# Performance work log

Hardware: AMD Instinct MI355X
Metric: run time of the kernel (lower is better)

The kernel has to match this reference:

```python
import jax, jax.numpy as jnp
import numpy as np

HIDDEN = 1024
INTER = 2048
NUM_EXPERTS = 8
TOPK = 2
STD = 0.02


def setup_inputs() -> dict:
    key = jax.random.key(0)
    k1, k2, k3, k4 = jax.random.split(key, 4)
    return {
        "hidden_states": jax.random.normal(k1, (1, 2048, HIDDEN), dtype=jnp.float32),
        "w1": jax.random.normal(k2, (NUM_EXPERTS, 2 * INTER, HIDDEN), dtype=jnp.float32) * STD,
        "w2": jax.random.normal(k3, (NUM_EXPERTS, HIDDEN, INTER), dtype=jnp.float32) * STD,
        "router_w": jax.random.normal(k4, (NUM_EXPERTS, HIDDEN), dtype=jnp.float32) * STD,
    }


def reference(hidden_states, w1, w2, router_w):
    # renormalize=False (the torch forward's default)
    orig_shape = hidden_states.shape
    dtype = hidden_states.dtype
    x = hidden_states.reshape(-1, orig_shape[-1])          # [T, H]
    E = w1.shape[0]

    gating = x @ router_w.T                                 # [T, E]
    probs = jax.nn.softmax(gating.astype(jnp.float32), axis=-1)
    topk_w, sel = jax.lax.top_k(probs, TOPK)                # [T, K]
    topk_w = topk_w.astype(dtype)

    # Per-(token, expert) combine weight; equivalent to the dispatch/sort/
    # grouped-GEMM/index_add path since unselected experts get weight 0.
    combine = (jax.nn.one_hot(sel, E, dtype=dtype) * topk_w[..., None]).sum(axis=1)  # [T, E]

    h = jnp.einsum('td,eid->tei', x, w1)                    # [T, E, 2*INTER]
    gate = jax.nn.silu(h[..., :INTER])
    y = h[..., INTER:] * gate                               # [T, E, INTER]
    out = jnp.einsum('tei,ehi,te->th', y, w2, combine)      # [T, H]
    return out.reshape(orig_shape)
```

## Files before the change

### kernel.cpp

```cpp
#include <hip/hip_runtime.h>
#include <hip/hip_bf16.h>
#include <math.h>

#define T_TOKENS 2048
#define HID 1024
#define INTER 2048
#define NE 8

typedef __attribute__((ext_vector_type(8))) __bf16 bf16x8;
typedef __attribute__((ext_vector_type(4))) __bf16 bf16x4;
typedef __attribute__((ext_vector_type(4))) float f32x4;

#define WS_COUNTS   0u
#define WS_OFFSETS  64u
#define WS_SEL      128u
#define WS_SELW     16512u
#define WS_ROWTOK   32896u
#define WS_ROWW     49280u
#define WS_TOKROWS  65664u
#define WS_XB       131072u
#define WS_Y        (131072u + 4194304u)
#define WS_Z        (131072u + 4194304u + 16777216u)

__device__ __forceinline__ void gload_lds16(const void* g, void* l) {
    __builtin_amdgcn_global_load_lds(
        (const __attribute__((address_space(1))) unsigned int*)g,
        (__attribute__((address_space(3))) unsigned int*)l, 16, 0, 0);
}

__device__ __forceinline__ bf16x8 cvt8(float4 a, float4 b) {
    bf16x8 r;
    r[0] = (__bf16)a.x; r[1] = (__bf16)a.y; r[2] = (__bf16)a.z; r[3] = (__bf16)a.w;
    r[4] = (__bf16)b.x; r[5] = (__bf16)b.y; r[6] = (__bf16)b.z; r[7] = (__bf16)b.w;
    return r;
}

__device__ __forceinline__ bf16x8 ldsfrag(const __bf16* base, int row, int c4) {
    return *(const bf16x8*)((const char*)base + row * 128 + ((c4 ^ (row & 7)) << 4));
}

__global__ __launch_bounds__(256) void moe_router(
    const float* __restrict__ x, const float* __restrict__ rw,
    int* __restrict__ counts, int* __restrict__ sel, float* __restrict__ selw,
    __bf16* __restrict__ xb)
{
    int wave = threadIdx.x >> 6;
    int lane = threadIdx.x & 63;
    int t = blockIdx.x * 4 + wave;
    if (t >= T_TOKENS) return;

    const float4* x4  = (const float4*)x + (size_t)t * (HID / 4);
    const float4* rw4 = (const float4*)rw;

    float acc[NE];
#pragma unroll
    for (int e = 0; e < NE; ++e) acc[e] = 0.f;
#pragma unroll
    for (int q = 0; q < 4; ++q) {
        int idx = q * 64 + lane;
        float4 xv = x4[idx];
        bf16x4 c;
        c[0] = (__bf16)xv.x; c[1] = (__bf16)xv.y; c[2] = (__bf16)xv.z; c[3] = (__bf16)xv.w;
        *(bf16x4*)(xb + (size_t)t * HID + idx * 4) = c;
#pragma unroll
        for (int e = 0; e < NE; ++e) {
            float4 rv = rw4[e * (HID / 4) + idx];
            acc[e] += xv.x * rv.x + xv.y * rv.y + xv.z * rv.z + xv.w * rv.w;
        }
    }
#pragma unroll
    for (int off = 32; off; off >>= 1)
#pragma unroll
        for (int e = 0; e < NE; ++e) acc[e] += __shfl_xor(acc[e], off, 64);

    if (lane == 0) {
        float m = acc[0];
#pragma unroll
        for (int e = 1; e < NE; ++e) m = fmaxf(m, acc[e]);
        float p[NE], s = 0.f;
#pragma unroll
        for (int e = 0; e < NE; ++e) { p[e] = expf(acc[e] - m); s += p[e]; }
        float inv = 1.f / s;
        int i0 = 0;
#pragma unroll
        for (int e = 1; e < NE; ++e) if (p[e] > p[i0]) i0 = e;
        int i1 = (i0 == 0) ? 1 : 0;
#pragma unroll
        for (int e = 0; e < NE; ++e) if (e != i0 && p[e] > p[i1]) i1 = e;
        sel[t * 2 + 0] = i0; selw[t * 2 + 0] = p[i0] * inv;
        sel[t * 2 + 1] = i1; selw[t * 2 + 1] = p[i1] * inv;
        atomicAdd(&counts[i0], 1);
        atomicAdd(&counts[i1], 1);
    }
}

__global__ __launch_bounds__(256) void moe_scan_assign(
    const int* __restrict__ counts, int* __restrict__ offsets,
    const int* __restrict__ sel, const float* __restrict__ selw,
    int* __restrict__ row_token, float* __restrict__ row_w,
    int* __restrict__ token_rows)
{
    __shared__ int soff[NE];
    __shared__ int scur[NE];
    if (threadIdx.x == 0) {
        int off = 0;
        for (int e = 0; e < NE; ++e) { soff[e] = off; off += counts[e]; }
    }
    if (threadIdx.x < NE) scur[threadIdx.x] = 0;
    __syncthreads();
    if (threadIdx.x < NE) offsets[threadIdx.x] = soff[threadIdx.x];
    for (int t = threadIdx.x; t < T_TOKENS; t += 256) {
#pragma unroll
        for (int k = 0; k < 2; ++k) {
            int e = sel[t * 2 + k];
            int slot = atomicAdd(&scur[e], 1);
            int r = soff[e] + slot;
            row_token[r] = t;
            row_w[r] = selw[t * 2 + k];
            token_rows[t * 2 + k] = r;
        }
    }
}

__global__ __launch_bounds__(256, 2) void moe_gemm1(
    const __bf16* __restrict__ xb, const float* __restrict__ w1,
    const int* __restrict__ row_token, const int* __restrict__ counts,
    const int* __restrict__ offsets, __bf16* __restrict__ y)
{
    int e = blockIdx.z;
    int cnt = counts[e];
    int row0 = blockIdx.y * 128;
    if (row0 >= cnt) return;
    int col0 = blockIdx.x * 64;
    int base = offsets[e];

    __shared__ __bf16 As[2][128 * 64];
    __shared__ __bf16 Bg[2][64 * 64];
    __shared__ __bf16 Bu[2][64 * 64];

    int tid = threadIdx.x;
    int lane = tid & 63;
    int wid = tid >> 6;
    int c4 = lane & 7;

    const __bf16* srcA[4];
    int dstA[4];
#pragma unroll
    for (int i = 0; i < 4; ++i) {
        int ii = wid * 4 + i;
        int r = ii * 8 + (lane >> 3);
        int rl = row0 + r; if (rl > cnt - 1) rl = cnt - 1;
        int tok = row_token[base + rl];
        srcA[i] = xb + (size_t)tok * HID + ((c4 ^ (r & 7)) << 3);
        dstA[i] = ii * 1024 + lane * 16;
    }
    const float* srcBg[2]; const float* srcBu[2]; int offB[2];
    int tc4 = tid & 7;
#pragma unroll
    for (int p = 0; p < 2; ++p) {
        int rb = p * 32 + (tid >> 3);
        srcBg[p] = w1 + ((size_t)e * 2 * INTER + col0 + rb) * HID + (tc4 << 3);
        srcBu[p] = srcBg[p] + (size_t)INTER * HID;
        offB[p] = rb * 128 + ((tc4 ^ (rb & 7)) << 4);
    }

#pragma unroll
    for (int i = 0; i < 4; ++i) gload_lds16(srcA[i], (char*)As[0] + dstA[i]);
#pragma unroll
    for (int p = 0; p < 2; ++p) {
        float4 g0 = *(const float4*)(srcBg[p]);
        float4 g1 = *(const float4*)(srcBg[p] + 4);
        float4 u0 = *(const float4*)(srcBu[p]);
        float4 u1 = *(const float4*)(srcBu[p] + 4);
        *(bf16x8*)((char*)Bg[0] + offB[p]) = cvt8(g0, g1);
        *(bf16x8*)((char*)Bu[0] + offB[p]) = cvt8(u0, u1);
    }
    __syncthreads();

    int wr = (wid >> 1) * 64, wc = (wid & 1) * 32;
    f32x4 ag[4][2] = {}, au[4][2] = {};

    for (int t = 0; t < 16; ++t) {
        int cur = t & 1;
        float4 g0[2], g1[2], u0[2], u1[2];
        bool pre = (t < 15);
        if (pre) {
            int k0 = (t + 1) * 64;
#pragma unroll
            for (int i = 0; i < 4; ++i)
                gload_lds16(srcA[i] + k0, (char*)As[cur ^ 1] + dstA[i]);
#pragma unroll
            for (int p = 0; p < 2; ++p) {
                g0[p] = *(const float4*)(srcBg[p] + k0);
                g1[p] = *(const float4*)(srcBg[p] + k0 + 4);
                u0[p] = *(const float4*)(srcBu[p] + k0);
                u1[p] = *(const float4*)(srcBu[p] + k0 + 4);
            }
        }
        const __bf16* Ab = As[cur];
        const __bf16* Bgb = Bg[cur];
        const __bf16* Bub = Bu[cur];
#pragma unroll
        for (int ks = 0; ks < 2; ++ks) {
            int kc4 = ks * 4 + (lane >> 4);
            bf16x8 a[4], bg[2], bu[2];
#pragma unroll
            for (int m = 0; m < 4; ++m) a[m] = ldsfrag(Ab, wr + m * 16 + (lane & 15), kc4);
#pragma unroll
            for (int n = 0; n < 2; ++n) {
                bg[n] = ldsfrag(Bgb, wc + n * 16 + (lane & 15), kc4);
                bu[n] = ldsfrag(Bub, wc + n * 16 + (lane & 15), kc4);
            }
#pragma unroll
            for (int m = 0; m < 4; ++m)
#pragma unroll
                for (int n = 0; n < 2; ++n) {
                    ag[m][n] = __builtin_amdgcn_mfma_f32_16x16x32_bf16(a[m], bg[n], ag[m][n], 0, 0, 0);
                    au[m][n] = __builtin_amdgcn_mfma_f32_16x16x32_bf16(a[m], bu[n], au[m][n], 0, 0, 0);
                }
        }
        if (pre) {
#pragma unroll
            for (int p = 0; p < 2; ++p) {
                *(bf16x8*)((char*)Bg[cur ^ 1] + offB[p]) = cvt8(g0[p], g1[p]);
                *(bf16x8*)((char*)Bu[cur ^ 1] + offB[p]) = cvt8(u0[p], u1[p]);
            }
        }
        __syncthreads();
    }

#pragma unroll
    for (int m = 0; m < 4; ++m) {
#pragma unroll
        for (int j = 0; j < 4; ++j) {
            int rl = wr + m * 16 + ((lane >> 4) << 2) + j;
            if (row0 + rl >= cnt) continue;
            size_t yrow = (size_t)(base + row0 + rl) * INTER;
#pragma unroll
            for (int n = 0; n < 2; ++n) {
                float g = ag[m][n][j], u = au[m][n][j];
                float s = g / (1.f + __expf(-g));
                y[yrow + col0 + wc + n * 16 + (lane & 15)] = (__bf16)(s * u);
            }
        }
    }
}

__global__ __launch_bounds__(256, 3) void moe_gemm2(
    const __bf16* __restrict__ y, const float* __restrict__ w2,
    const float* __restrict__ row_w, const int* __restrict__ counts,
    const int* __restrict__ offsets, float* __restrict__ z)
{
    int e = blockIdx.z;
    int cnt = counts[e];
    int row0 = blockIdx.y * 128;
    if (row0 >= cnt) return;
    int col0 = blockIdx.x * 64;
    int base = offsets[e];

    __shared__ __bf16 As[2][128 * 64];
    __shared__ __bf16 Bs[2][64 * 64];

    int tid = threadIdx.x;
    int lane = tid & 63;
    int wid = tid >> 6;
    int c4 = lane & 7;

    const __bf16* srcA[4];
    int dstA[4];
#pragma unroll
    for (int i = 0; i < 4; ++i) {
        int ii = wid * 4 + i;
        int r = ii * 8 + (lane >> 3);
        int rl = row0 + r; if (rl > cnt - 1) rl = cnt - 1;
        srcA[i] = y + (size_t)(base + rl) * INTER + ((c4 ^ (r & 7)) << 3);
        dstA[i] = ii * 1024 + lane * 16;
    }
    const float* srcB[2]; int offB[2];
    int tc4 = tid & 7;
#pragma unroll
    for (int p = 0; p < 2; ++p) {
        int rb = p * 32 + (tid >> 3);
        srcB[p] = w2 + ((size_t)e * HID + col0 + rb) * INTER + (tc4 << 3);
        offB[p] = rb * 128 + ((tc4 ^ (rb & 7)) << 4);
    }

#pragma unroll
    for (int i = 0; i < 4; ++i) gload_lds16(srcA[i], (char*)As[0] + dstA[i]);
#pragma unroll
    for (int p = 0; p < 2; ++p) {
        float4 b0 = *(const float4*)(srcB[p]);
        float4 b1 = *(const float4*)(srcB[p] + 4);
        *(bf16x8*)((char*)Bs[0] + offB[p]) = cvt8(b0, b1);
    }
    __syncthreads();

    int wr = (wid >> 1) * 64, wc = (wid & 1) * 32;
    f32x4 acc[4][2] = {};

    for (int t = 0; t < 32; ++t) {
        int cur = t & 1;
        float4 b0[2], b1[2];
        bool pre = (t < 31);
        if (pre) {
            int k0 = (t + 1) * 64;
#pragma unroll
            for (int i = 0; i < 4; ++i)
                gload_lds16(srcA[i] + k0, (char*)As[cur ^ 1] + dstA[i]);
#pragma unroll
            for (int p = 0; p < 2; ++p) {
                b0[p] = *(const float4*)(srcB[p] + k0);
                b1[p] = *(const float4*)(srcB[p] + k0 + 4);
            }
        }
        const __bf16* Ab = As[cur];
        const __bf16* Bb = Bs[cur];
#pragma unroll
        for (int ks = 0; ks < 2; ++ks) {
            int kc4 = ks * 4 + (lane >> 4);
            bf16x8 a[4], b[2];
#pragma unroll
            for (int m = 0; m < 4; ++m) a[m] = ldsfrag(Ab, wr + m * 16 + (lane & 15), kc4);
#pragma unroll
            for (int n = 0; n < 2; ++n) b[n] = ldsfrag(Bb, wc + n * 16 + (lane & 15), kc4);
#pragma unroll
            for (int m = 0; m < 4; ++m)
#pragma unroll
                for (int n = 0; n < 2; ++n)
                    acc[m][n] = __builtin_amdgcn_mfma_f32_16x16x32_bf16(a[m], b[n], acc[m][n], 0, 0, 0);
        }
        if (pre) {
#pragma unroll
            for (int p = 0; p < 2; ++p)
                *(bf16x8*)((char*)Bs[cur ^ 1] + offB[p]) = cvt8(b0[p], b1[p]);
        }
        __syncthreads();
    }

#pragma unroll
    for (int m = 0; m < 4; ++m) {
#pragma unroll
        for (int j = 0; j < 4; ++j) {
            int rl = wr + m * 16 + ((lane >> 4) << 2) + j;
            if (row0 + rl >= cnt) continue;
            float wgt = row_w[base + row0 + rl];
            size_t zrow = (size_t)(base + row0 + rl) * HID;
#pragma unroll
            for (int n = 0; n < 2; ++n)
                z[zrow + col0 + wc + n * 16 + (lane & 15)] = acc[m][n][j] * wgt;
        }
    }
}

__global__ __launch_bounds__(256) void moe_combine(
    const float* __restrict__ z, const int* __restrict__ token_rows,
    float* __restrict__ out)
{
    int total = T_TOKENS * (HID / 4);
    for (int idx = blockIdx.x * 256 + threadIdx.x; idx < total; idx += gridDim.x * 256) {
        int t  = idx >> 8;
        int h4 = idx & 255;
        int r0 = token_rows[t * 2 + 0];
        int r1 = token_rows[t * 2 + 1];
        const float4* z4 = (const float4*)z;
        float4 a = z4[(size_t)r0 * 256 + h4];
        float4 b = z4[(size_t)r1 * 256 + h4];
        float4 o = {a.x + b.x, a.y + b.y, a.z + b.z, a.w + b.w};
        ((float4*)out)[(size_t)t * 256 + h4] = o;
    }
}

extern "C" void kernel_launch(void* const* d_in, const int* in_sizes, int n_in,
                              void* d_out, int out_size, void* d_ws, size_t ws_size,
                              hipStream_t stream) {
    const float* x  = (const float*)d_in[0];
    const float* w1 = (const float*)d_in[1];
    const float* w2 = (const float*)d_in[2];
    const float* rw = (const float*)d_in[3];
    float* out = (float*)d_out;

    char* ws = (char*)d_ws;
    int*    counts     = (int*)(ws + WS_COUNTS);
    int*    offsets    = (int*)(ws + WS_OFFSETS);
    int*    sel        = (int*)(ws + WS_SEL);
    float*  selw       = (float*)(ws + WS_SELW);
    int*    row_token  = (int*)(ws + WS_ROWTOK);
    float*  row_w      = (float*)(ws + WS_ROWW);
    int*    token_rows = (int*)(ws + WS_TOKROWS);
    __bf16* xb         = (__bf16*)(ws + WS_XB);
    __bf16* y          = (__bf16*)(ws + WS_Y);
    float*  z          = (float*)(ws + WS_Z);

    hipMemsetAsync(ws, 0, 128, stream);

    moe_router<<<T_TOKENS / 4, 256, 0, stream>>>(x, rw, counts, sel, selw, xb);
    moe_scan_assign<<<1, 256, 0, stream>>>(counts, offsets, sel, selw,
                                           row_token, row_w, token_rows);
    moe_gemm1<<<dim3(INTER / 64, 16, NE), 256, 0, stream>>>(
        xb, w1, row_token, counts, offsets, y);
    moe_gemm2<<<dim3(HID / 64, 16, NE), 256, 0, stream>>>(
        y, w2, row_w, counts, offsets, z);
    moe_combine<<<1024, 256, 0, stream>>>(z, token_rows, out);
}
```

Before: 407.7 us.

## Fuse combine into gemm2 via atomics, split-K gemm2, halve K tile

```diff
diff --git a/kernel.cpp b/kernel.cpp
--- a/kernel.cpp
+++ b/kernel.cpp
@@ -17,10 +17,8 @@
 #define WS_SELW     16512u
 #define WS_ROWTOK   32896u
 #define WS_ROWW     49280u
-#define WS_TOKROWS  65664u
 #define WS_XB       131072u
 #define WS_Y        (131072u + 4194304u)
-#define WS_Z        (131072u + 4194304u + 16777216u)
 
 __device__ __forceinline__ void gload_lds16(const void* g, void* l) {
     __builtin_amdgcn_global_load_lds(
@@ -35,8 +33,9 @@
     return r;
 }
 
-__device__ __forceinline__ bf16x8 ldsfrag(const __bf16* base, int row, int c4) {
-    return *(const bf16x8*)((const char*)base + row * 128 + ((c4 ^ (row & 7)) << 4));
+__device__ __forceinline__ bf16x8 ldsfrag(const __bf16* base, int row, int g) {
+    return *(const bf16x8*)((const char*)base + row * 64 +
+                            ((g ^ ((row >> 1) & 3)) << 4));
 }
 
 __global__ __launch_bounds__(256) void moe_router(
@@ -97,8 +96,7 @@
 __global__ __launch_bounds__(256) void moe_scan_assign(
     const int* __restrict__ counts, int* __restrict__ offsets,
     const int* __restrict__ sel, const float* __restrict__ selw,
-    int* __restrict__ row_token, float* __restrict__ row_w,
-    int* __restrict__ token_rows)
+    int* __restrict__ row_token, float* __restrict__ row_w)
 {
     __shared__ int soff[NE];
     __shared__ int scur[NE];
@@ -117,12 +115,11 @@
             int r = soff[e] + slot;
             row_token[r] = t;
             row_w[r] = selw[t * 2 + k];
-            token_rows[t * 2 + k] = r;
-        }
-    }
-}
-
-__global__ __launch_bounds__(256, 2) void moe_gemm1(
+        }
+    }
+}
+
+__global__ __launch_bounds__(256, 4) void moe_gemm1(
     const __bf16* __restrict__ xb, const float* __restrict__ w1,
     const int* __restrict__ row_token, const int* __restrict__ counts,
     const int* __restrict__ offsets, __bf16* __restrict__ y)
@@ -134,82 +131,72 @@
     int col0 = blockIdx.x * 64;
     int base = offsets[e];
 
-    __shared__ __bf16 As[2][128 * 64];
-    __shared__ __bf16 Bg[2][64 * 64];
-    __shared__ __bf16 Bu[2][64 * 64];
+    __shared__ __bf16 As[2][128 * 32];
+    __shared__ __bf16 Bg[2][64 * 32];
+    __shared__ __bf16 Bu[2][64 * 32];
 
     int tid = threadIdx.x;
     int lane = tid & 63;
     int wid = tid >> 6;
-    int c4 = lane & 7;
-
-    const __bf16* srcA[4];
-    int dstA[4];
-#pragma unroll
-    for (int i = 0; i < 4; ++i) {
-        int ii = wid * 4 + i;
-        int r = ii * 8 + (lane >> 3);
+    int gq = tid & 3;
+    int sw = (tid >> 3) & 3;
+
+    const __bf16* srcA[2];
+    int dstA[2];
+#pragma unroll
+    for (int i = 0; i < 2; ++i) {
+        int r = i * 64 + (tid >> 2);
         int rl = row0 + r; if (rl > cnt - 1) rl = cnt - 1;
         int tok = row_token[base + rl];
-        srcA[i] = xb + (size_t)tok * HID + ((c4 ^ (r & 7)) << 3);
-        dstA[i] = ii * 1024 + lane * 16;
-    }
-    const float* srcBg[2]; const float* srcBu[2]; int offB[2];
-    int tc4 = tid & 7;
-#pragma unroll
-    for (int p = 0; p < 2; ++p) {
-        int rb = p * 32 + (tid >> 3);
-        srcBg[p] = w1 + ((size_t)e * 2 * INTER + col0 + rb) * HID + (tc4 << 3);
-        srcBu[p] = srcBg[p] + (size_t)INTER * HID;
-        offB[p] = rb * 128 + ((tc4 ^ (rb & 7)) << 4);
-    }
-
-#pragma unroll
-    for (int i = 0; i < 4; ++i) gload_lds16(srcA[i], (char*)As[0] + dstA[i]);
-#pragma unroll
-    for (int p = 0; p < 2; ++p) {
-        float4 g0 = *(const float4*)(srcBg[p]);
-        float4 g1 = *(const float4*)(srcBg[p] + 4);
-        float4 u0 = *(const float4*)(srcBu[p]);
-        float4 u1 = *(const float4*)(srcBu[p] + 4);
-        *(bf16x8*)((char*)Bg[0] + offB[p]) = cvt8(g0, g1);
-        *(bf16x8*)((char*)Bu[0] + offB[p]) = cvt8(u0, u1);
+        srcA[i] = xb + (size_t)tok * HID + ((gq ^ sw) << 3);
+        dstA[i] = i * 4096 + tid * 16;
+    }
+    int rb = tid >> 2;
+    const float* srcBg = w1 + ((size_t)e * 2 * INTER + col0 + rb) * HID + (gq << 3);
+    const float* srcBu = srcBg + (size_t)INTER * HID;
+    int offB = rb * 64 + ((gq ^ sw) << 4);
+
+#pragma unroll
+    for (int i = 0; i < 2; ++i) gload_lds16(srcA[i], (char*)As[0] + dstA[i]);
+    {
+        float4 g0 = *(const float4*)(srcBg);
+        float4 g1 = *(const float4*)(srcBg + 4);
+        float4 u0 = *(const float4*)(srcBu);
+        float4 u1 = *(const float4*)(srcBu + 4);
+        *(bf16x8*)((char*)Bg[0] + offB) = cvt8(g0, g1);
+        *(bf16x8*)((char*)Bu[0] + offB) = cvt8(u0, u1);
     }
     __syncthreads();
 
     int wr = (wid >> 1) * 64, wc = (wid & 1) * 32;
     f32x4 ag[4][2] = {}, au[4][2] = {};
 
-    for (int t = 0; t < 16; ++t) {
+    for (int t = 0; t < 32; ++t) {
         int cur = t & 1;
-        float4 g0[2], g1[2], u0[2], u1[2];
-        bool pre = (t < 15);
+        float4 g0, g1, u0, u1;
+        bool pre = (t < 31);
         if (pre) {
-            int k0 = (t + 1) * 64;
-#pragma unroll
-            for (int i = 0; i < 4; ++i)
+            int k0 = (t + 1) * 32;
+#pragma unroll
+            for (int i = 0; i < 2; ++i)
                 gload_lds16(srcA[i] + k0, (char*)As[cur ^ 1] + dstA[i]);
-#pragma unroll
-            for (int p = 0; p < 2; ++p) {
-                g0[p] = *(const float4*)(srcBg[p] + k0);
-                g1[p] = *(const float4*)(srcBg[p] + k0 + 4);
-                u0[p] = *(const float4*)(srcBu[p] + k0);
-                u1[p] = *(const float4*)(srcBu[p] + k0 + 4);
-            }
+            g0 = *(const float4*)(srcBg + k0);
+            g1 = *(const float4*)(srcBg + k0 + 4);
+            u0 = *(const float4*)(srcBu + k0);
+            u1 = *(const float4*)(srcBu + k0 + 4);
         }
         const __bf16* Ab = As[cur];
         const __bf16* Bgb = Bg[cur];
         const __bf16* Bub = Bu[cur];
-#pragma unroll
-        for (int ks = 0; ks < 2; ++ks) {
-            int kc4 = ks * 4 + (lane >> 4);
+        {
+            int kg = lane >> 4;
             bf16x8 a[4], bg[2], bu[2];
 #pragma unroll
-            for (int m = 0; m < 4; ++m) a[m] = ldsfrag(Ab, wr + m * 16 + (lane & 15), kc4);
+            for (int m = 0; m < 4; ++m) a[m] = ldsfrag(Ab, wr + m * 16 + (lane & 15), kg);
 #pragma unroll
             for (int n = 0; n < 2; ++n) {
-                bg[n] = ldsfrag(Bgb, wc + n * 16 + (lane & 15), kc4);
-                bu[n] = ldsfrag(Bub, wc + n * 16 + (lane & 15), kc4);
+                bg[n] = ldsfrag(Bgb, wc + n * 16 + (lane & 15), kg);
+                bu[n] = ldsfrag(Bub, wc + n * 16 + (lane & 15), kg);
             }
 #pragma unroll
             for (int m = 0; m < 4; ++m)
@@ -220,11 +207,8 @@
                 }
         }
         if (pre) {
-#pragma unroll
-            for (int p = 0; p < 2; ++p) {
-                *(bf16x8*)((char*)Bg[cur ^ 1] + offB[p]) = cvt8(g0[p], g1[p]);
-                *(bf16x8*)((char*)Bu[cur ^ 1] + offB[p]) = cvt8(u0[p], u1[p]);
-            }
+            *(bf16x8*)((char*)Bg[cur ^ 1] + offB) = cvt8(g0, g1);
+            *(bf16x8*)((char*)Bu[cur ^ 1] + offB) = cvt8(u0, u1);
         }
         __syncthreads();
     }
@@ -246,52 +230,48 @@
     }
 }
 
-__global__ __launch_bounds__(256, 3) void moe_gemm2(
+__global__ __launch_bounds__(256, 4) void moe_gemm2(
     const __bf16* __restrict__ y, const float* __restrict__ w2,
-    const float* __restrict__ row_w, const int* __restrict__ counts,
-    const int* __restrict__ offsets, float* __restrict__ z)
+    const float* __restrict__ row_w, const int* __restrict__ row_token,
+    const int* __restrict__ counts, const int* __restrict__ offsets,
+    float* __restrict__ out)
 {
     int e = blockIdx.z;
     int cnt = counts[e];
-    int row0 = blockIdx.y * 128;
+    int row0 = (blockIdx.y >> 1) * 128;
     if (row0 >= cnt) return;
+    int kbase = (blockIdx.y & 1) * (INTER / 2);
     int col0 = blockIdx.x * 64;
     int base = offsets[e];
 
-    __shared__ __bf16 As[2][128 * 64];
-    __shared__ __bf16 Bs[2][64 * 64];
+    __shared__ __bf16 As[2][128 * 32];
+    __shared__ __bf16 Bs[2][64 * 32];
 
     int tid = threadIdx.x;
     int lane = tid & 63;
     int wid = tid >> 6;
-    int c4 = lane & 7;
-
-    const __bf16* srcA[4];
-    int dstA[4];
-#pragma unroll
-    for (int i = 0; i < 4; ++i) {
-        int ii = wid * 4 + i;
-        int r = ii * 8 + (lane >> 3);
+    int gq = tid & 3;
+    int sw = (tid >> 3) & 3;
+
+    const __bf16* srcA[2];
+    int dstA[2];
+#pragma unroll
+    for (int i = 0; i < 2; ++i) {
+        int r = i * 64 + (tid >> 2);
         int rl = row0 + r; if (rl > cnt - 1) rl = cnt - 1;
-        srcA[i] = y + (size_t)(base + rl) * INTER + ((c4 ^ (r & 7)) << 3);
-        dstA[i] = ii * 1024 + lane * 16;
-    }
-    const float* srcB[2]; int offB[2];
-    int tc4 = tid & 7;
-#pragma unroll
-    for (int p = 0; p < 2; ++p) {
-        int rb = p * 32 + (tid >> 3);
-        srcB[p] = w2 + ((size_t)e * HID + col0 + rb) * INTER + (tc4 << 3);
-        offB[p] = rb * 128 + ((tc4 ^ (rb & 7)) << 4);
-    }
-
-#pragma unroll
-    for (int i = 0; i < 4; ++i) gload_lds16(srcA[i], (char*)As[0] + dstA[i]);
-#pragma unroll
-    for (int p = 0; p < 2; ++p) {
-        float4 b0 = *(const float4*)(srcB[p]);
-        float4 b1 = *(const float4*)(srcB[p] + 4);
-        *(bf16x8*)((char*)Bs[0] + offB[p]) = cvt8(b0, b1);
+        srcA[i] = y + (size_t)(base + rl) * INTER + kbase + ((gq ^ sw) << 3);
+        dstA[i] = i * 4096 + tid * 16;
+    }
+    int rb = tid >> 2;
+    const float* srcB = w2 + ((size_t)e * HID + col0 + rb) * INTER + kbase + (gq << 3);
+    int offB = rb * 64 + ((gq ^ sw) << 4);
+
+#pragma unroll
+    for (int i = 0; i < 2; ++i) gload_lds16(srcA[i], (char*)As[0] + dstA[i]);
+    {
+        float4 b0 = *(const float4*)(srcB);
+        float4 b1 = *(const float4*)(srcB + 4);
+        *(bf16x8*)((char*)Bs[0] + offB) = cvt8(b0, b1);
     }
     __syncthreads();
 
@@ -300,29 +280,25 @@
 
     for (int t = 0; t < 32; ++t) {
         int cur = t & 1;
-        float4 b0[2], b1[2];
+        float4 b0, b1;
         bool pre = (t < 31);
         if (pre) {
-            int k0 = (t + 1) * 64;
-#pragma unroll
-            for (int i = 0; i < 4; ++i)
+            int k0 = (t + 1) * 32;
+#pragma unroll
+            for (int i = 0; i < 2; ++i)
                 gload_lds16(srcA[i] + k0, (char*)As[cur ^ 1] + dstA[i]);
-#pragma unroll
-            for (int p = 0; p < 2; ++p) {
-                b0[p] = *(const float4*)(srcB[p] + k0);
-                b1[p] = *(const float4*)(srcB[p] + k0 + 4);
-            }
+            b0 = *(const float4*)(srcB + k0);
+            b1 = *(const float4*)(srcB + k0 + 4);
         }
         const __bf16* Ab = As[cur];
         const __bf16* Bb = Bs[cur];
-#pragma unroll
-        for (int ks = 0; ks < 2; ++ks) {
-            int kc4 = ks * 4 + (lane >> 4);
+        {
+            int kg = lane >> 4;
             bf16x8 a[4], b[2];
 #pragma unroll
-            for (int m = 0; m < 4; ++m) a[m] = ldsfrag(Ab, wr + m * 16 + (lane & 15), kc4);
-#pragma unroll
-            for (int n = 0; n < 2; ++n) b[n] = ldsfrag(Bb, wc + n * 16 + (lane & 15), kc4);
+            for (int m = 0; m < 4; ++m) a[m] = ldsfrag(Ab, wr + m * 16 + (lane & 15), kg);
+#pragma unroll
+            for (int n = 0; n < 2; ++n) b[n] = ldsfrag(Bb, wc + n * 16 + (lane & 15), kg);
 #pragma unroll
             for (int m = 0; m < 4; ++m)
 #pragma unroll
@@ -330,9 +306,7 @@
                     acc[m][n] = __builtin_amdgcn_mfma_f32_16x16x32_bf16(a[m], b[n], acc[m][n], 0, 0, 0);
         }
         if (pre) {
-#pragma unroll
-            for (int p = 0; p < 2; ++p)
-                *(bf16x8*)((char*)Bs[cur ^ 1] + offB[p]) = cvt8(b0[p], b1[p]);
+            *(bf16x8*)((char*)Bs[cur ^ 1] + offB) = cvt8(b0, b1);
         }
         __syncthreads();
     }
@@ -344,29 +318,12 @@
             int rl = wr + m * 16 + ((lane >> 4) << 2) + j;
             if (row0 + rl >= cnt) continue;
             float wgt = row_w[base + row0 + rl];
-            size_t zrow = (size_t)(base + row0 + rl) * HID;
+            int tok = row_token[base + row0 + rl];
 #pragma unroll
             for (int n = 0; n < 2; ++n)
-                z[zrow + col0 + wc + n * 16 + (lane & 15)] = acc[m][n][j] * wgt;
-        }
-    }
-}
-
-__global__ __launch_bounds__(256) void moe_combine(
-    const float* __restrict__ z, const int* __restrict__ token_rows,
-    float* __restrict__ out)
-{
-    int total = T_TOKENS * (HID / 4);
-    for (int idx = blockIdx.x * 256 + threadIdx.x; idx < total; idx += gridDim.x * 256) {
-        int t  = idx >> 8;
-        int h4 = idx & 255;
-        int r0 = token_rows[t * 2 + 0];
-        int r1 = token_rows[t * 2 + 1];
-        const float4* z4 = (const float4*)z;
-        float4 a = z4[(size_t)r0 * 256 + h4];
-        float4 b = z4[(size_t)r1 * 256 + h4];
-        float4 o = {a.x + b.x, a.y + b.y, a.z + b.z, a.w + b.w};
-        ((float4*)out)[(size_t)t * 256 + h4] = o;
+                atomicAdd(&out[(size_t)tok * HID + col0 + wc + n * 16 + (lane & 15)],
+                          acc[m][n][j] * wgt);
+        }
     }
 }
 
@@ -386,19 +343,17 @@
     float*  selw       = (float*)(ws + WS_SELW);
     int*    row_token  = (int*)(ws + WS_ROWTOK);
     float*  row_w      = (float*)(ws + WS_ROWW);
-    int*    token_rows = (int*)(ws + WS_TOKROWS);
     __bf16* xb         = (__bf16*)(ws + WS_XB);
     __bf16* y          = (__bf16*)(ws + WS_Y);
-    float*  z          = (float*)(ws + WS_Z);
 
     hipMemsetAsync(ws, 0, 128, stream);
+    hipMemsetAsync(out, 0, (size_t)T_TOKENS * HID * sizeof(float), stream);
 
     moe_router<<<T_TOKENS / 4, 256, 0, stream>>>(x, rw, counts, sel, selw, xb);
     moe_scan_assign<<<1, 256, 0, stream>>>(counts, offsets, sel, selw,
-                                           row_token, row_w, token_rows);
+                                           row_token, row_w);
     moe_gemm1<<<dim3(INTER / 64, 16, NE), 256, 0, stream>>>(
         xb, w1, row_token, counts, offsets, y);
-    moe_gemm2<<<dim3(HID / 64, 16, NE), 256, 0, stream>>>(
-        y, w2, row_w, counts, offsets, z);
-    moe_combine<<<1024, 256, 0, stream>>>(z, token_rows, out);
-}
+    moe_gemm2<<<dim3(HID / 64, 32, NE), 256, 0, stream>>>(
+        y, w2, row_w, row_token, counts, offsets, out);
+}
```

Result: slower. 423.8 us (+3.9%).
